# Performance work log

Measured on AMD Instinct MI355X. Metric: run time of the kernel, lower is better.

The kernel has to match this reference:

```python
import jax, jax.numpy as jnp
import numpy as np

VOCAB = 32000
EMB = 512
T = 20  # sentence_max_length
B = 64


def setup_inputs() -> dict:
    key = jax.random.key(0)
    ks = jax.random.split(key, 8)
    features = jax.random.normal(ks[0], (B, EMB), dtype=jnp.float32)
    captions = jax.random.randint(ks[1], (B, T), 0, VOCAB)
    W_emb = jax.random.normal(ks[2], (VOCAB, EMB), dtype=jnp.float32) * 0.02
    W_out = jax.random.normal(ks[3], (VOCAB, EMB), dtype=jnp.float32) * 0.02
    b_out = jnp.zeros((VOCAB,), dtype=jnp.float32)
    # LSTM params (PyTorch layout: [4*H, in], gate order i, f, g, o)
    W_ih = jax.random.normal(ks[4], (4 * EMB, EMB), dtype=jnp.float32) * (1.0 / np.sqrt(EMB))
    W_hh = jax.random.normal(ks[5], (4 * EMB, EMB), dtype=jnp.float32) * (1.0 / np.sqrt(EMB))
    b_ih = jnp.zeros((4 * EMB,), dtype=jnp.float32)
    b_hh = jnp.zeros((4 * EMB,), dtype=jnp.float32)
    return {"features": features, "captions": captions, "W_emb": W_emb,
            "W_out": W_out, "b_out": b_out, "W_ih": W_ih, "W_hh": W_hh,
            "b_ih": b_ih, "b_hh": b_hh}


def _lstm_scan(emb_steps, h0, c0, W_ih, W_hh, b_ih, b_hh):
    # emb_steps: [T-1, B, E]; returns stacked hidden states [T-1, B, E]
    def cell(carry, x):
        h, c = carry
        gates = x @ W_ih.T + b_ih + h @ W_hh.T + b_hh  # [B, 4E]
        i, f, g, o = jnp.split(gates, 4, axis=-1)
        i, f, o = jax.nn.sigmoid(i), jax.nn.sigmoid(f), jax.nn.sigmoid(o)
        g = jnp.tanh(g)
        c = f * c + i * g
        h = o * jnp.tanh(c)
        return (h, c), h

    (_, _), hs = jax.lax.scan(cell, (h0, c0), emb_steps)
    return hs


def reference(features, captions, W_emb, W_out, b_out, W_ih, W_hh, b_ih, b_hh):
    # Teacher-forced decode. h0 = zeros, c0 = features (per original code).
    emb = W_emb[captions]  # [B, T, E]
    h0 = jnp.zeros_like(features)
    c0 = features
    # Step i (i=1..T-1) consumes embedding of captions[:, i-1]
    xs = jnp.swapaxes(emb[:, : T - 1], 0, 1)  # [T-1, B, E]
    hs = _lstm_scan(xs, h0, c0, W_ih, W_hh, b_ih, b_hh)  # [T-1, B, E]
    hs = jnp.swapaxes(hs, 0, 1)  # [B, T-1, E]
    # out[0] = Linear(Embed(captions[:,0])); out[i] = Linear(h_i)
    seq = jnp.concatenate([emb[:, :1], hs], axis=1)  # [B, T, E]
    logits = jnp.einsum("bte,ve->btv", seq, W_out) + b_out  # [B, T, V]
    return logits
```

## Files before the change

kernel.cpp:

```cpp
#include <hip/hip_runtime.h>
#include <hip/hip_bf16.h>

#define Bb 64
#define Tt 20
#define Ee 512
#define Vv 32000
#define NB 32

typedef __hip_bfloat16 bf16;
typedef __attribute__((ext_vector_type(8))) short bf16x8;
typedef __attribute__((ext_vector_type(4))) float f32x4;

__device__ __forceinline__ bf16 f2bf(float x) { return __float2bfloat16(x); }

__global__ void convert_w(const float* __restrict__ src, bf16* __restrict__ dst) {
  int i = blockIdx.x * blockDim.x + threadIdx.x;
  float4 v = ((const float4*)src)[i];
  union { ushort4 u; bf16 h[4]; } pk;
  pk.h[0] = f2bf(v.x); pk.h[1] = f2bf(v.y); pk.h[2] = f2bf(v.z); pk.h[3] = f2bf(v.w);
  ((ushort4*)dst)[i] = pk.u;
}

__global__ void embed_init(const int* __restrict__ caps, const float* __restrict__ Wemb,
                           bf16* __restrict__ emb, bf16* __restrict__ seq,
                           unsigned int* __restrict__ bar) {
  int row = blockIdx.x;
  int t = row % Tt;
  int tid = threadIdx.x;
  if (row == 0) {
    for (int i = tid; i < NB * 16 + Tt; i += 128) bar[i] = 0;
  }
  int tok = caps[row];
  float4 v = ((const float4*)(Wemb + (size_t)tok * Ee))[tid];
  union { ushort4 u; bf16 h[4]; } pk;
  pk.h[0] = f2bf(v.x); pk.h[1] = f2bf(v.y); pk.h[2] = f2bf(v.z); pk.h[3] = f2bf(v.w);
  ((ushort4*)(emb + (size_t)row * Ee))[tid] = pk.u;
  if (t == 0) ((ushort4*)(seq + (size_t)row * Ee))[tid] = pk.u;
}

__global__ __launch_bounds__(512) void xproj(
    const bf16* __restrict__ A,
    const bf16* __restrict__ Bw,
    const float* __restrict__ bih, const float* __restrict__ bhh,
    float* __restrict__ gx)
{
  __shared__ __align__(16) bf16 Bs[8][64][16][8];
  int tid = threadIdx.x;
  int lane = tid & 63;
  int quad = lane >> 4, ln = lane & 15;
  int wid = tid >> 6;
  int wm = wid & 1, wn = wid >> 1;
  int n0 = blockIdx.x * 128, m0 = blockIdx.y * 128;

#pragma unroll
  for (int q = 0; q < 16; ++q) {
    int c = q * 512 + tid;
    int r = c >> 6, k8 = c & 63;
    *(uint4*)&Bs[r >> 4][k8][r & 15][0] =
        *(const uint4*)(Bw + (size_t)(n0 + r) * Ee + k8 * 8);
  }
  __syncthreads();

  f32x4 zero = {0.f, 0.f, 0.f, 0.f};
  f32x4 acc[4][2];
#pragma unroll
  for (int mt = 0; mt < 4; ++mt)
#pragma unroll
    for (int nt = 0; nt < 2; ++nt) acc[mt][nt] = zero;

  const bf16* Abase = A + (size_t)(m0 + wm * 64 + ln) * Ee;
#pragma unroll 4
  for (int kk = 0; kk < 16; ++kk) {
    int k = kk * 32 + quad * 8;
    bf16x8 af[4], bfv[2];
#pragma unroll
    for (int mt = 0; mt < 4; ++mt)
      af[mt] = *(const bf16x8*)(Abase + (size_t)mt * 16 * Ee + k);
#pragma unroll
    for (int nt = 0; nt < 2; ++nt)
      bfv[nt] = *(const bf16x8*)&Bs[wn * 2 + nt][kk * 4 + quad][ln][0];
#pragma unroll
    for (int mt = 0; mt < 4; ++mt)
#pragma unroll
      for (int nt = 0; nt < 2; ++nt)
        acc[mt][nt] = __builtin_amdgcn_mfma_f32_16x16x32_bf16(af[mt], bfv[nt], acc[mt][nt], 0, 0, 0);
  }

#pragma unroll
  for (int nt = 0; nt < 2; ++nt) {
    int col = n0 + wn * 32 + nt * 16 + ln;
    float bsum = bih[col] + bhh[col];
#pragma unroll
    for (int mt = 0; mt < 4; ++mt) {
#pragma unroll
      for (int r = 0; r < 4; ++r) {
        int row = m0 + wm * 64 + mt * 16 + quad * 4 + r;
        gx[(size_t)row * (4 * Ee) + col] = acc[mt][nt][r] + bsum;
      }
    }
  }
}

__global__ __launch_bounds__(256) void lstm_rec(
    const float* __restrict__ gx,
    bf16* __restrict__ seq,
    const float* __restrict__ feats,
    const bf16* __restrict__ Whh,
    unsigned int* __restrict__ bar)
{
  const long XS = (long)Tt * Ee;
  __shared__ __align__(16) bf16 wl[4][64][16][8];
  __shared__ float gsm[4][64][17];

  int tid = threadIdx.x;
  int g = tid >> 6;
  int lane = tid & 63;
  int quad = lane >> 4, ln = lane & 15;
  int j0 = blockIdx.x * 16;
  int bid = blockIdx.x;
  unsigned int* goflags = bar + NB * 16;

#pragma unroll
  for (int q = 0; q < 16; ++q) {
    int c = q * 256 + tid;
    int row = c >> 6, k8 = c & 63;
    int gg = row >> 4, rr = row & 15;
    *(uint4*)&wl[gg][k8][rr][0] =
        *(const uint4*)(Whh + ((size_t)gg * Ee + j0 + rr) * Ee + k8 * 8);
  }

  int bq = tid >> 2;
  int jq = (tid & 3) * 4;
  const float* gxb = gx + (size_t)bq * Tt * (4 * Ee) + j0 + jq;

  f32x4 creg = *(const f32x4*)(feats + (size_t)bq * Ee + j0 + jq);

  f32x4 pre[4];
#pragma unroll
  for (int gg = 0; gg < 4; ++gg) pre[gg] = *(const f32x4*)(gxb + gg * Ee);
  __syncthreads();

  for (int t = 1; t < Tt; ++t) {
    if (t > 1) {
      const bf16* hb = seq + (size_t)(t - 1) * Ee;
      f32x4 zero = {0.f, 0.f, 0.f, 0.f};
      f32x4 acc[4];
#pragma unroll
      for (int mt = 0; mt < 4; ++mt) acc[mt] = zero;
#pragma unroll 4
      for (int kk = 0; kk < 16; ++kk) {
        int k = kk * 32 + quad * 8;
        bf16x8 bfrag = *(const bf16x8*)&wl[g][kk * 4 + quad][ln][0];
#pragma unroll
        for (int mt = 0; mt < 4; ++mt) {
          bf16x8 afrag = *(const bf16x8*)(hb + (size_t)(mt * 16 + ln) * XS + k);
          acc[mt] = __builtin_amdgcn_mfma_f32_16x16x32_bf16(afrag, bfrag, acc[mt], 0, 0, 0);
        }
      }
#pragma unroll
      for (int mt = 0; mt < 4; ++mt)
#pragma unroll
        for (int r = 0; r < 4; ++r)
          gsm[g][mt * 16 + quad * 4 + r][ln] = acc[mt][r];
    }
    __syncthreads();

    union { ushort4 u; bf16 h[4]; } st;
#pragma unroll
    for (int jj = 0; jj < 4; ++jj) {
      int jl = jq + jj;
      float iv = pre[0][jj];
      float fv = pre[1][jj];
      float gv = pre[2][jj];
      float ov = pre[3][jj];
      if (t > 1) {
        iv += gsm[0][bq][jl];
        fv += gsm[1][bq][jl];
        gv += gsm[2][bq][jl];
        ov += gsm[3][bq][jl];
      }
      iv = 1.f / (1.f + __expf(-iv));
      fv = 1.f / (1.f + __expf(-fv));
      ov = 1.f / (1.f + __expf(-ov));
      gv = tanhf(gv);
      creg[jj] = fv * creg[jj] + iv * gv;
      st.h[jj] = f2bf(ov * tanhf(creg[jj]));
    }
    *(ushort4*)(seq + (size_t)bq * XS + (size_t)t * Ee + j0 + jq) = st.u;

    if (t < Tt - 1) {
#pragma unroll
      for (int gg = 0; gg < 4; ++gg)
        pre[gg] = *(const f32x4*)(gxb + (size_t)t * (4 * Ee) + gg * Ee);

      __syncthreads();
      if (tid == 0)
        __hip_atomic_store(&bar[bid * 16], (unsigned)t, __ATOMIC_RELEASE,
                           __HIP_MEMORY_SCOPE_AGENT);
      if (bid == 0) {
        if (tid < 64) {
          for (;;) {
            unsigned v = (tid < NB)
                ? __hip_atomic_load(&bar[tid * 16], __ATOMIC_RELAXED,
                                    __HIP_MEMORY_SCOPE_AGENT)
                : (unsigned)t;
            if (__all(v == (unsigned)t)) break;
            __builtin_amdgcn_s_sleep(2);
          }
          if (tid == 0)
            __hip_atomic_store(&goflags[t], (unsigned)t, __ATOMIC_RELEASE,
                               __HIP_MEMORY_SCOPE_AGENT);
        }
      } else if (tid == 0) {
        while (__hip_atomic_load(&goflags[t], __ATOMIC_RELAXED,
                                 __HIP_MEMORY_SCOPE_AGENT) != (unsigned)t)
          __builtin_amdgcn_s_sleep(2);
      }
      if (tid == 0)
        (void)__hip_atomic_load(&goflags[t], __ATOMIC_ACQUIRE,
                                __HIP_MEMORY_SCOPE_AGENT);
      __syncthreads();
    }
  }
}

__global__ __launch_bounds__(512) void out_gemm(
    const bf16* __restrict__ A,
    const float* __restrict__ Bw,
    const float* __restrict__ bias,
    float* __restrict__ Cb)
{
  __shared__ __align__(16) bf16 Bs[8][64][16][8];
  int tid = threadIdx.x;
  int lane = tid & 63;
  int quad = lane >> 4, ln = lane & 15;
  int wid = tid >> 6;
  int wm = wid & 1, wn = wid >> 1;
  int n0 = blockIdx.x * 128;

#pragma unroll
  for (int q = 0; q < 16; ++q) {
    int c = q * 512 + tid;
    int r = c >> 6, k8 = c & 63;
    const float* src = Bw + (size_t)(n0 + r) * Ee + k8 * 8;
    float4 f0 = *(const float4*)src;
    float4 f1 = *(const float4*)(src + 4);
    union { uint4 u; bf16 h[8]; } pk;
    pk.h[0] = f2bf(f0.x); pk.h[1] = f2bf(f0.y); pk.h[2] = f2bf(f0.z); pk.h[3] = f2bf(f0.w);
    pk.h[4] = f2bf(f1.x); pk.h[5] = f2bf(f1.y); pk.h[6] = f2bf(f1.z); pk.h[7] = f2bf(f1.w);
    *(uint4*)&Bs[r >> 4][k8][r & 15][0] = pk.u;
  }
  __syncthreads();

  float bv[2];
#pragma unroll
  for (int nt = 0; nt < 2; ++nt) bv[nt] = bias[n0 + wn * 32 + nt * 16 + ln];

  for (int m0 = 0; m0 < Bb * Tt; m0 += 128) {
    f32x4 zero = {0.f, 0.f, 0.f, 0.f};
    f32x4 acc[4][2];
#pragma unroll
    for (int mt = 0; mt < 4; ++mt)
#pragma unroll
      for (int nt = 0; nt < 2; ++nt) acc[mt][nt] = zero;

    const bf16* Abase = A + (size_t)(m0 + wm * 64 + ln) * Ee;
#pragma unroll 4
    for (int kk = 0; kk < 16; ++kk) {
      int k = kk * 32 + quad * 8;
      bf16x8 af[4], bfv[2];
#pragma unroll
      for (int mt = 0; mt < 4; ++mt)
        af[mt] = *(const bf16x8*)(Abase + (size_t)mt * 16 * Ee + k);
#pragma unroll
      for (int nt = 0; nt < 2; ++nt)
        bfv[nt] = *(const bf16x8*)&Bs[wn * 2 + nt][kk * 4 + quad][ln][0];
#pragma unroll
      for (int mt = 0; mt < 4; ++mt)
#pragma unroll
        for (int nt = 0; nt < 2; ++nt)
          acc[mt][nt] = __builtin_amdgcn_mfma_f32_16x16x32_bf16(af[mt], bfv[nt], acc[mt][nt], 0, 0, 0);
    }

#pragma unroll
    for (int mt = 0; mt < 4; ++mt) {
#pragma unroll
      for (int nt = 0; nt < 2; ++nt) {
        int col = n0 + wn * 32 + nt * 16 + ln;
#pragma unroll
        for (int r = 0; r < 4; ++r) {
          int row = m0 + wm * 64 + mt * 16 + quad * 4 + r;
          Cb[(size_t)row * Vv + col] = acc[mt][nt][r] + bv[nt];
        }
      }
    }
  }
}

extern "C" void kernel_launch(void* const* d_in, const int* in_sizes, int n_in,
                              void* d_out, int out_size, void* d_ws, size_t ws_size,
                              hipStream_t stream) {
  (void)in_sizes; (void)n_in; (void)out_size; (void)ws_size;
  const float* feats = (const float*)d_in[0];
  const int*   caps  = (const int*)d_in[1];
  const float* Wemb  = (const float*)d_in[2];
  const float* Wout  = (const float*)d_in[3];
  const float* bout  = (const float*)d_in[4];
  const float* Wih   = (const float*)d_in[5];
  const float* Whh   = (const float*)d_in[6];
  const float* bih   = (const float*)d_in[7];
  const float* bhh   = (const float*)d_in[8];
  float* out = (float*)d_out;

  bf16* emb    = (bf16*)d_ws;
  bf16* seq    = emb   + (size_t)Bb * Tt * Ee;
  bf16* Wih_b  = seq   + (size_t)Bb * Tt * Ee;
  bf16* Whh_b  = Wih_b + (size_t)4 * Ee * Ee;
  float* gx    = (float*)(Whh_b + (size_t)4 * Ee * Ee);
  unsigned int* bar = (unsigned int*)(gx + (size_t)Bb * Tt * 4 * Ee);

  const int WN4 = (4 * Ee * Ee) / 4;
  convert_w<<<WN4 / 256, 256, 0, stream>>>(Wih, Wih_b);
  convert_w<<<WN4 / 256, 256, 0, stream>>>(Whh, Whh_b);
  embed_init<<<Bb * Tt, 128, 0, stream>>>(caps, Wemb, emb, seq, bar);
  xproj<<<dim3(16, 10), 512, 0, stream>>>(emb, Wih_b, bih, bhh, gx);
  lstm_rec<<<NB, 256, 0, stream>>>(gx, seq, feats, Whh_b, bar);
  out_gemm<<<dim3(Vv / 128), 512, 0, stream>>>(seq, Wout, bout, out);
}
```

Before: 632.5 us.

## Retile GEMMs with K-looped LDS tiles, XCD-aware out_gemm grid, flat LSTM barrier

The output GEMM goes from 250 blocks that each loop over all M tiles to 2560 blocks of 128x128 tiles, mapped so each XCD gets contiguous vocab bands. A, converted W_out and xproj inputs are now staged through LDS in BK=64 chunks, with four waves each computing 64x64. The LSTM recurrence replaces the two-level master/go-flag barrier with a flat barrier where every block polls all flags, using relaxed atomics for h loads and stores. The aim is more parallelism and less barrier latency, at the cost of re-reading and converting W_out fp32 for each of the 10 M tiles and relying on weaker memory ordering.

```diff
diff --git a/kernel.cpp b/kernel.cpp
--- a/kernel.cpp
+++ b/kernel.cpp
@@ -38,13 +38,14 @@
   if (t == 0) ((ushort4*)(seq + (size_t)row * Ee))[tid] = pk.u;
 }
 
-__global__ __launch_bounds__(512) void xproj(
+__global__ __launch_bounds__(256) void xproj(
     const bf16* __restrict__ A,
     const bf16* __restrict__ Bw,
     const float* __restrict__ bih, const float* __restrict__ bhh,
     float* __restrict__ gx)
 {
-  __shared__ __align__(16) bf16 Bs[8][64][16][8];
+  __shared__ __align__(16) bf16 As[128 * 64];
+  __shared__ __align__(16) bf16 Bs[128 * 64];
   int tid = threadIdx.x;
   int lane = tid & 63;
   int quad = lane >> 4, ln = lane & 15;
@@ -52,43 +53,53 @@
   int wm = wid & 1, wn = wid >> 1;
   int n0 = blockIdx.x * 128, m0 = blockIdx.y * 128;
 
-#pragma unroll
-  for (int q = 0; q < 16; ++q) {
-    int c = q * 512 + tid;
-    int r = c >> 6, k8 = c & 63;
-    *(uint4*)&Bs[r >> 4][k8][r & 15][0] =
-        *(const uint4*)(Bw + (size_t)(n0 + r) * Ee + k8 * 8);
-  }
-  __syncthreads();
-
   f32x4 zero = {0.f, 0.f, 0.f, 0.f};
-  f32x4 acc[4][2];
+  f32x4 acc[4][4];
 #pragma unroll
   for (int mt = 0; mt < 4; ++mt)
 #pragma unroll
-    for (int nt = 0; nt < 2; ++nt) acc[mt][nt] = zero;
-
-  const bf16* Abase = A + (size_t)(m0 + wm * 64 + ln) * Ee;
-#pragma unroll 4
-  for (int kk = 0; kk < 16; ++kk) {
-    int k = kk * 32 + quad * 8;
-    bf16x8 af[4], bfv[2];
-#pragma unroll
-    for (int mt = 0; mt < 4; ++mt)
-      af[mt] = *(const bf16x8*)(Abase + (size_t)mt * 16 * Ee + k);
-#pragma unroll
-    for (int nt = 0; nt < 2; ++nt)
-      bfv[nt] = *(const bf16x8*)&Bs[wn * 2 + nt][kk * 4 + quad][ln][0];
-#pragma unroll
-    for (int mt = 0; mt < 4; ++mt)
-#pragma unroll
-      for (int nt = 0; nt < 2; ++nt)
-        acc[mt][nt] = __builtin_amdgcn_mfma_f32_16x16x32_bf16(af[mt], bfv[nt], acc[mt][nt], 0, 0, 0);
-  }
-
-#pragma unroll
-  for (int nt = 0; nt < 2; ++nt) {
-    int col = n0 + wn * 32 + nt * 16 + ln;
+    for (int nt = 0; nt < 4; ++nt) acc[mt][nt] = zero;
+
+  for (int k0 = 0; k0 < Ee; k0 += 64) {
+    uint4 avv[4], bvv[4];
+#pragma unroll
+    for (int q = 0; q < 4; ++q) {
+      int fb = (q * 256 + tid) * 16;
+      int row = fb >> 7;
+      int cb = fb & 127;
+      avv[q] = *(const uint4*)((const char*)A + ((size_t)(m0 + row) * Ee + k0) * 2 + cb);
+      bvv[q] = *(const uint4*)((const char*)Bw + ((size_t)(n0 + row) * Ee + k0) * 2 + cb);
+    }
+#pragma unroll
+    for (int q = 0; q < 4; ++q) {
+      int fb = (q * 256 + tid) * 16;
+      *(uint4*)((char*)As + fb) = avv[q];
+      *(uint4*)((char*)Bs + fb) = bvv[q];
+    }
+    __syncthreads();
+
+#pragma unroll
+    for (int kk = 0; kk < 2; ++kk) {
+      int kb = (kk * 32 + quad * 8) * 2;
+      bf16x8 af[4], bfv[4];
+#pragma unroll
+      for (int mt = 0; mt < 4; ++mt)
+        af[mt] = *(const bf16x8*)((const char*)As + (wm * 64 + mt * 16 + ln) * 128 + kb);
+#pragma unroll
+      for (int nt = 0; nt < 4; ++nt)
+        bfv[nt] = *(const bf16x8*)((const char*)Bs + (wn * 64 + nt * 16 + ln) * 128 + kb);
+#pragma unroll
+      for (int mt = 0; mt < 4; ++mt)
+#pragma unroll
+        for (int nt = 0; nt < 4; ++nt)
+          acc[mt][nt] = __builtin_amdgcn_mfma_f32_16x16x32_bf16(af[mt], bfv[nt], acc[mt][nt], 0, 0, 0);
+    }
+    __syncthreads();
+  }
+
+#pragma unroll
+  for (int nt = 0; nt < 4; ++nt) {
+    int col = n0 + wn * 64 + nt * 16 + ln;
     float bsum = bih[col] + bhh[col];
 #pragma unroll
     for (int mt = 0; mt < 4; ++mt) {
@@ -118,7 +129,6 @@
   int quad = lane >> 4, ln = lane & 15;
   int j0 = blockIdx.x * 16;
   int bid = blockIdx.x;
-  unsigned int* goflags = bar + NB * 16;
 
 #pragma unroll
   for (int q = 0; q < 16; ++q) {
@@ -142,7 +152,7 @@
 
   for (int t = 1; t < Tt; ++t) {
     if (t > 1) {
-      const bf16* hb = seq + (size_t)(t - 1) * Ee;
+      bf16* hb = seq + (size_t)(t - 1) * Ee;
       f32x4 zero = {0.f, 0.f, 0.f, 0.f};
       f32x4 acc[4];
 #pragma unroll
@@ -153,8 +163,12 @@
         bf16x8 bfrag = *(const bf16x8*)&wl[g][kk * 4 + quad][ln][0];
 #pragma unroll
         for (int mt = 0; mt < 4; ++mt) {
-          bf16x8 afrag = *(const bf16x8*)(hb + (size_t)(mt * 16 + ln) * XS + k);
-          acc[mt] = __builtin_amdgcn_mfma_f32_16x16x32_bf16(afrag, bfrag, acc[mt], 0, 0, 0);
+          union { unsigned long long q[2]; bf16x8 v; } hl;
+          unsigned long long* hp =
+              (unsigned long long*)(hb + (size_t)(mt * 16 + ln) * XS + k);
+          hl.q[0] = __hip_atomic_load(hp, __ATOMIC_RELAXED, __HIP_MEMORY_SCOPE_AGENT);
+          hl.q[1] = __hip_atomic_load(hp + 1, __ATOMIC_RELAXED, __HIP_MEMORY_SCOPE_AGENT);
+          acc[mt] = __builtin_amdgcn_mfma_f32_16x16x32_bf16(hl.v, bfrag, acc[mt], 0, 0, 0);
         }
       }
 #pragma unroll
@@ -165,7 +179,7 @@
     }
     __syncthreads();
 
-    union { ushort4 u; bf16 h[4]; } st;
+    union { ushort4 u; unsigned long long q; bf16 h[4]; } st;
 #pragma unroll
     for (int jj = 0; jj < 4; ++jj) {
       int jl = jq + jj;
@@ -186,7 +200,9 @@
       creg[jj] = fv * creg[jj] + iv * gv;
       st.h[jj] = f2bf(ov * tanhf(creg[jj]));
     }
-    *(ushort4*)(seq + (size_t)bq * XS + (size_t)t * Ee + j0 + jq) = st.u;
+    __hip_atomic_store(
+        (unsigned long long*)(seq + (size_t)bq * XS + (size_t)t * Ee + j0 + jq),
+        st.q, __ATOMIC_RELAXED, __HIP_MEMORY_SCOPE_AGENT);
 
     if (t < Tt - 1) {
 #pragma unroll
@@ -195,103 +211,106 @@
 
       __syncthreads();
       if (tid == 0)
-        __hip_atomic_store(&bar[bid * 16], (unsigned)t, __ATOMIC_RELEASE,
+        __hip_atomic_store(&bar[bid * 16], (unsigned)t, __ATOMIC_RELAXED,
                            __HIP_MEMORY_SCOPE_AGENT);
-      if (bid == 0) {
-        if (tid < 64) {
-          for (;;) {
-            unsigned v = (tid < NB)
-                ? __hip_atomic_load(&bar[tid * 16], __ATOMIC_RELAXED,
-                                    __HIP_MEMORY_SCOPE_AGENT)
-                : (unsigned)t;
-            if (__all(v == (unsigned)t)) break;
-            __builtin_amdgcn_s_sleep(2);
-          }
-          if (tid == 0)
-            __hip_atomic_store(&goflags[t], (unsigned)t, __ATOMIC_RELEASE,
-                               __HIP_MEMORY_SCOPE_AGENT);
-        }
-      } else if (tid == 0) {
-        while (__hip_atomic_load(&goflags[t], __ATOMIC_RELAXED,
-                                 __HIP_MEMORY_SCOPE_AGENT) != (unsigned)t)
-          __builtin_amdgcn_s_sleep(2);
-      }
-      if (tid == 0)
-        (void)__hip_atomic_load(&goflags[t], __ATOMIC_ACQUIRE,
-                                __HIP_MEMORY_SCOPE_AGENT);
+      if (tid < NB) {
+        while (__hip_atomic_load(&bar[tid * 16], __ATOMIC_RELAXED,
+                                 __HIP_MEMORY_SCOPE_AGENT) < (unsigned)t)
+          __builtin_amdgcn_s_sleep(1);
+      }
       __syncthreads();
     }
   }
 }
 
-__global__ __launch_bounds__(512) void out_gemm(
-    const bf16* __restrict__ A,
-    const float* __restrict__ Bw,
-    const float* __restrict__ bias,
-    float* __restrict__ Cb)
-{
-  __shared__ __align__(16) bf16 Bs[8][64][16][8];
+#define BM 128
+#define BN 128
+#define BK 64
+
+__global__ __launch_bounds__(256) void out_gemm(const bf16* __restrict__ A,
+                                                const float* __restrict__ Bw,
+                                                const float* __restrict__ bias,
+                                                float* __restrict__ Cb) {
+  __shared__ __align__(16) bf16 As[BM * BK];
+  __shared__ __align__(16) bf16 Bs[BN * BK];
+  int bid = blockIdx.x;
+  int xcd = bid & 7, slot = bid >> 3;
+  int mi = slot % 10, grp = slot / 10;
+  int band = grp * 8 + xcd;
+  if (band >= Vv / BN) return;
+  int m0 = mi * BM, n0 = band * BN;
+
   int tid = threadIdx.x;
   int lane = tid & 63;
   int quad = lane >> 4, ln = lane & 15;
   int wid = tid >> 6;
   int wm = wid & 1, wn = wid >> 1;
-  int n0 = blockIdx.x * 128;
-
-#pragma unroll
-  for (int q = 0; q < 16; ++q) {
-    int c = q * 512 + tid;
-    int r = c >> 6, k8 = c & 63;
-    const float* src = Bw + (size_t)(n0 + r) * Ee + k8 * 8;
-    float4 f0 = *(const float4*)src;
-    float4 f1 = *(const float4*)(src + 4);
-    union { uint4 u; bf16 h[8]; } pk;
-    pk.h[0] = f2bf(f0.x); pk.h[1] = f2bf(f0.y); pk.h[2] = f2bf(f0.z); pk.h[3] = f2bf(f0.w);
-    pk.h[4] = f2bf(f1.x); pk.h[5] = f2bf(f1.y); pk.h[6] = f2bf(f1.z); pk.h[7] = f2bf(f1.w);
-    *(uint4*)&Bs[r >> 4][k8][r & 15][0] = pk.u;
-  }
-  __syncthreads();
-
-  float bv[2];
-#pragma unroll
-  for (int nt = 0; nt < 2; ++nt) bv[nt] = bias[n0 + wn * 32 + nt * 16 + ln];
-
-  for (int m0 = 0; m0 < Bb * Tt; m0 += 128) {
-    f32x4 zero = {0.f, 0.f, 0.f, 0.f};
-    f32x4 acc[4][2];
-#pragma unroll
-    for (int mt = 0; mt < 4; ++mt)
-#pragma unroll
-      for (int nt = 0; nt < 2; ++nt) acc[mt][nt] = zero;
-
-    const bf16* Abase = A + (size_t)(m0 + wm * 64 + ln) * Ee;
-#pragma unroll 4
-    for (int kk = 0; kk < 16; ++kk) {
-      int k = kk * 32 + quad * 8;
-      bf16x8 af[4], bfv[2];
-#pragma unroll
-      for (int mt = 0; mt < 4; ++mt)
-        af[mt] = *(const bf16x8*)(Abase + (size_t)mt * 16 * Ee + k);
-#pragma unroll
-      for (int nt = 0; nt < 2; ++nt)
-        bfv[nt] = *(const bf16x8*)&Bs[wn * 2 + nt][kk * 4 + quad][ln][0];
-#pragma unroll
-      for (int mt = 0; mt < 4; ++mt)
-#pragma unroll
-        for (int nt = 0; nt < 2; ++nt)
+
+  f32x4 zero = {0.f, 0.f, 0.f, 0.f};
+  f32x4 acc[4][4];
+#pragma unroll
+  for (int mt = 0; mt < 4; ++mt)
+#pragma unroll
+    for (int nt = 0; nt < 4; ++nt) acc[mt][nt] = zero;
+
+  for (int k0 = 0; k0 < Ee; k0 += BK) {
+    uint4 avv[4];
+    float4 bf0[4], bf1[4];
+#pragma unroll
+    for (int q = 0; q < 4; ++q) {
+      int fb = (q * 256 + tid) * 16;
+      int row = fb >> 7;
+      int c8 = (fb & 127) >> 1;
+      avv[q] = *(const uint4*)((const char*)A + ((size_t)(m0 + row) * Ee + k0) * 2 + (fb & 127));
+      const float* src = Bw + (size_t)(n0 + row) * Ee + k0 + c8;
+      bf0[q] = *(const float4*)(src);
+      bf1[q] = *(const float4*)(src + 4);
+    }
+#pragma unroll
+    for (int q = 0; q < 4; ++q) {
+      int fb = (q * 256 + tid) * 16;
+      *(uint4*)((char*)As + fb) = avv[q];
+      union { uint4 u; bf16 h[8]; } pk;
+      pk.h[0] = f2bf(bf0[q].x); pk.h[1] = f2bf(bf0[q].y);
+      pk.h[2] = f2bf(bf0[q].z); pk.h[3] = f2bf(bf0[q].w);
+      pk.h[4] = f2bf(bf1[q].x); pk.h[5] = f2bf(bf1[q].y);
+      pk.h[6] = f2bf(bf1[q].z); pk.h[7] = f2bf(bf1[q].w);
+      *(uint4*)((char*)Bs + fb) = pk.u;
+    }
+    __syncthreads();
+
+#pragma unroll
+    for (int kk = 0; kk < 2; ++kk) {
+      int kb = (kk * 32 + quad * 8) * 2;
+      bf16x8 af[4], bfv[4];
+#pragma unroll
+      for (int mt = 0; mt < 4; ++mt)
+        af[mt] = *(const bf16x8*)((const char*)As + (wm * 64 + mt * 16 + ln) * 128 + kb);
+#pragma unroll
+      for (int nt = 0; nt < 4; ++nt)
+        bfv[nt] = *(const bf16x8*)((const char*)Bs + (wn * 64 + nt * 16 + ln) * 128 + kb);
+#pragma unroll
+      for (int mt = 0; mt < 4; ++mt)
+#pragma unroll
+        for (int nt = 0; nt < 4; ++nt)
           acc[mt][nt] = __builtin_amdgcn_mfma_f32_16x16x32_bf16(af[mt], bfv[nt], acc[mt][nt], 0, 0, 0);
     }
-
-#pragma unroll
-    for (int mt = 0; mt < 4; ++mt) {
-#pragma unroll
-      for (int nt = 0; nt < 2; ++nt) {
-        int col = n0 + wn * 32 + nt * 16 + ln;
-#pragma unroll
-        for (int r = 0; r < 4; ++r) {
-          int row = m0 + wm * 64 + mt * 16 + quad * 4 + r;
-          Cb[(size_t)row * Vv + col] = acc[mt][nt][r] + bv[nt];
-        }
+    __syncthreads();
+  }
+
+  float bv[4];
+#pragma unroll
+  for (int nt = 0; nt < 4; ++nt)
+    bv[nt] = bias[n0 + wn * 64 + nt * 16 + ln];
+#pragma unroll
+  for (int mt = 0; mt < 4; ++mt) {
+#pragma unroll
+    for (int nt = 0; nt < 4; ++nt) {
+      int col = n0 + wn * 64 + nt * 16 + ln;
+#pragma unroll
+      for (int r = 0; r < 4; ++r) {
+        int row = m0 + wm * 64 + mt * 16 + quad * 4 + r;
+        Cb[(size_t)row * Vv + col] = acc[mt][nt][r] + bv[nt];
       }
     }
   }
@@ -323,7 +342,7 @@
   convert_w<<<WN4 / 256, 256, 0, stream>>>(Wih, Wih_b);
   convert_w<<<WN4 / 256, 256, 0, stream>>>(Whh, Whh_b);
   embed_init<<<Bb * Tt, 128, 0, stream>>>(caps, Wemb, emb, seq, bar);
-  xproj<<<dim3(16, 10), 512, 0, stream>>>(emb, Wih_b, bih, bhh, gx);
+  xproj<<<dim3(16, 10), 256, 0, stream>>>(emb, Wih_b, bih, bhh, gx);
   lstm_rec<<<NB, 256, 0, stream>>>(gx, seq, feats, Whh_b, bar);
-  out_gemm<<<dim3(Vv / 128), 512, 0, stream>>>(seq, Wout, bout, out);
-}
+  out_gemm<<<2560, 256, 0, stream>>>(seq, Wout, bout, out);
+}
```

After: 674.3 us. 1.07x slower.
